# Optimization experiments

Hardware: AMD Instinct MI355X
Metric: run time of the kernel (lower is better)

Reference implementation:

```python
import jax, jax.numpy as jnp
import numpy as np

D_MODEL = 1024
L_MAX = 2048
BATCH = 4
ORDER = 2
FILTER_ORDER = 64
EMB_DIM = 3            # HyenaFilter default positional-embedding dim
SHORT_K = 3
HEAD_DIM = D_MODEL     # num_heads = 1
TOTAL_WIDTH = D_MODEL * (ORDER + 1)
# ExponentialModulation constants (Safari defaults)
MAX_DECAY = np.log(1e-2) / 0.3
MIN_DECAY = np.log(1e-2) / 1.5


def setup_inputs() -> dict:
    key = jax.random.key(0)
    ks = jax.random.split(key, 12)
    s = 0.02
    return {
        "u": jax.random.normal(ks[0], (BATCH, L_MAX, D_MODEL), jnp.float32),
        "in_w": jax.random.normal(ks[1], (D_MODEL, TOTAL_WIDTH), jnp.float32) * s,
        "in_b": jnp.zeros((TOTAL_WIDTH,), jnp.float32),
        "short_w": jax.random.normal(ks[2], (TOTAL_WIDTH, 1, SHORT_K), jnp.float32) * 0.3,
        "short_b": jnp.zeros((TOTAL_WIDTH,), jnp.float32),
        "mlp_w0": jax.random.normal(ks[3], (EMB_DIM, FILTER_ORDER), jnp.float32) * 0.4,
        "mlp_b0": jnp.zeros((FILTER_ORDER,), jnp.float32),
        "freq0": 10.0 * jnp.ones((1, FILTER_ORDER), jnp.float32),
        "mlp_w1": jax.random.normal(ks[4], (FILTER_ORDER, FILTER_ORDER), jnp.float32) * 0.12,
        "mlp_b1": jnp.zeros((FILTER_ORDER,), jnp.float32),
        "freq1": 10.0 * jnp.ones((1, FILTER_ORDER), jnp.float32),
        "mlp_w2": jax.random.normal(ks[5], (FILTER_ORDER, FILTER_ORDER), jnp.float32) * 0.12,
        "mlp_b2": jnp.zeros((FILTER_ORDER,), jnp.float32),
        "freq2": 10.0 * jnp.ones((1, FILTER_ORDER), jnp.float32),
        "mlp_w3": jax.random.normal(ks[6], (FILTER_ORDER, HEAD_DIM), jnp.float32) * 0.1,
        "filter_bias": jax.random.normal(ks[7], (HEAD_DIM,), jnp.float32),
        "out_w": jax.random.normal(ks[8], (D_MODEL, D_MODEL), jnp.float32) * s,
        "out_b": jnp.zeros((D_MODEL,), jnp.float32),
    }


def _pos_emb(L):
    # PositionalEmbedding: t in [0,1], plus exp(-1j * f * w) real/imag bands
    bands = (EMB_DIM - 1) // 2
    t = jnp.linspace(0.0, 1.0, L, dtype=jnp.float32)[:, None]                # (L, 1)
    w = 2.0 * jnp.pi * jnp.linspace(0.0, L - 1.0, L, dtype=jnp.float32)[:, None] / L
    f = jnp.linspace(1e-4, float(bands - 1), bands, dtype=jnp.float32)[None, :]
    phase = f * w                                                             # (L, bands)
    # exp(-1j*phase): real = cos(phase), imag = -sin(phase)
    z = jnp.concatenate([t, jnp.cos(phase), -jnp.sin(phase)], axis=-1)        # (L, EMB_DIM)
    return z, t


def _implicit_filter(L, mlp_w0, mlp_b0, freq0, mlp_w1, mlp_b1, freq1,
                     mlp_w2, mlp_b2, freq2, mlp_w3):
    z, t = _pos_emb(L)
    h = jnp.sin(freq0 * (z @ mlp_w0 + mlp_b0))
    h = jnp.sin(freq1 * (h @ mlp_w1 + mlp_b1))
    h = jnp.sin(freq2 * (h @ mlp_w2 + mlp_b2))
    h = h @ mlp_w3                                                            # (L, HEAD_DIM)
    # ExponentialModulation (shift = 0)
    deltas = jnp.linspace(MIN_DECAY, MAX_DECAY, HEAD_DIM, dtype=jnp.float32)[None, :]
    h = h * jnp.exp(-t * jnp.abs(deltas))
    return h                                                                  # (L, HEAD_DIM)


def _fftconv(u, k, bias):
    # u: (b, v, L), k: (v, L), bias: (v,) -- causal linear conv via 2L FFT
    L = u.shape[-1]
    n = 2 * L
    k_f = jnp.fft.rfft(k, n=n) / n                                            # (v, n//2+1)
    u_f = jnp.fft.rfft(u, n=n)                                                # (b, v, n//2+1)
    y = jnp.fft.irfft(u_f * k_f, n=n, norm="forward")[..., :L]
    return y + u * bias[:, None]


def reference(u, in_w, in_b, short_w, short_b,
              mlp_w0, mlp_b0, freq0, mlp_w1, mlp_b1, freq1,
              mlp_w2, mlp_b2, freq2, mlp_w3, filter_bias, out_w, out_b):
    b, l, d = u.shape
    up = u @ in_w + in_b                                                      # (b, l, 3d)
    up = jnp.transpose(up, (0, 2, 1))                                         # (b, 3d, l)
    # depthwise causal short conv (torch pad=k-1 both sides then [:l] == left pad only)
    uc = jax.lax.conv_general_dilated(
        up, short_w, window_strides=(1,), padding=[(SHORT_K - 1, 0)],
        dimension_numbers=("NCH", "OIH", "NCH"), feature_group_count=TOTAL_WIDTH)
    uc = uc + short_b[None, :, None]                                          # (b, 3d, l)
    x0, x1, v = jnp.split(uc, ORDER + 1, axis=1)                              # each (b, d, l)
    k = _implicit_filter(l, mlp_w0, mlp_b0, freq0, mlp_w1, mlp_b1, freq1,
                         mlp_w2, mlp_b2, freq2, mlp_w3).T                     # (d, l)
    v = v * x1                                                                # gate
    v = _fftconv(v, k, filter_bias)                                           # long conv
    y = jnp.transpose(v * x0, (0, 2, 1))                                      # (b, l, d)
    return y @ out_w + out_b
```

## Files before the change

kernel.cpp:

```cpp
#include <hip/hip_runtime.h>
#include <stdint.h>

typedef unsigned short u16;
typedef __attribute__((ext_vector_type(8))) short short8;
typedef __attribute__((ext_vector_type(4))) short short4x;
typedef __attribute__((ext_vector_type(4))) float f32x4;

#define PI_F 3.14159265358979323846f
#define L_SEQ 2048
#define NFFT 4096
#define DM 1024
#define TW 3072
#define BATCH 4

__device__ __forceinline__ u16 f2bf(float f){
  union { float f; uint32_t u; } v; v.f = f;
  uint32_t r = v.u + 0x7fffu + ((v.u >> 16) & 1u);
  return (u16)(r >> 16);
}
__device__ __forceinline__ float bf2f(u16 h){
  union { uint32_t u; float f; } v; v.u = ((uint32_t)h) << 16;
  return v.f;
}

__device__ __forceinline__ void async16(const void* g, void* l){
  __builtin_amdgcn_global_load_lds(
      (const __attribute__((address_space(1))) void*)g,
      (__attribute__((address_space(3))) void*)l, 16, 0, 0);
}

__device__ __forceinline__ void sincos_rev(float rev, float& sn, float& cs){
  asm("v_sin_f32 %0, %1" : "=v"(sn) : "v"(rev));
  asm("v_cos_f32 %0, %1" : "=v"(cs) : "v"(rev));
}

__device__ __forceinline__ float2 cmulf(float2 a, float c, float s){
  return make_float2(a.x*c - a.y*s, a.x*s + a.y*c);
}

__device__ __forceinline__ int P16(int i){ return i + (i >> 4); }

__device__ static constexpr int BR4[16] = {0,8,4,12,2,10,6,14,1,9,5,13,3,11,7,15};

template<int SGN>
__device__ __forceinline__ void fft16(float2* a){
  const float s = (float)SGN;
  static constexpr float tc[8]  = {1.f, 0.92387953f, 0.70710678f, 0.38268343f,
                                   0.f, -0.38268343f, -0.70710678f, -0.92387953f};
  static constexpr float ts_[8] = {0.f, -0.38268343f, -0.70710678f, -0.92387953f,
                                   -1.f, -0.92387953f, -0.70710678f, -0.38268343f};
  #pragma unroll
  for (int j = 0; j < 8; ++j){
    float2 u = a[j], v = a[j+8];
    float2 d = make_float2(u.x - v.x, u.y - v.y);
    a[j] = make_float2(u.x + v.x, u.y + v.y);
    a[j+8] = cmulf(d, tc[j], s*ts_[j]);
  }
  #pragma unroll
  for (int g = 0; g < 2; ++g){
    int b = g*8;
    #pragma unroll
    for (int j = 0; j < 4; ++j){
      float2 u = a[b+j], v = a[b+j+4];
      float2 d = make_float2(u.x - v.x, u.y - v.y);
      a[b+j] = make_float2(u.x + v.x, u.y + v.y);
      a[b+j+4] = cmulf(d, tc[2*j], s*ts_[2*j]);
    }
  }
  #pragma unroll
  for (int g = 0; g < 4; ++g){
    int b = g*4;
    #pragma unroll
    for (int j = 0; j < 2; ++j){
      float2 u = a[b+j], v = a[b+j+2];
      float2 d = make_float2(u.x - v.x, u.y - v.y);
      a[b+j] = make_float2(u.x + v.x, u.y + v.y);
      a[b+j+2] = (j == 0) ? d : cmulf(d, 0.f, -s);
    }
  }
  #pragma unroll
  for (int g = 0; g < 8; ++g){
    int b = g*2;
    float2 u = a[b], v = a[b+1];
    a[b] = make_float2(u.x + v.x, u.y + v.y);
    a[b+1] = make_float2(u.x - v.x, u.y - v.y);
  }
}

__global__ void k_convert_u(const float4* __restrict__ in, u16* __restrict__ outp, int n4){
  int idx = blockIdx.x * blockDim.x + threadIdx.x;
  int stride = gridDim.x * blockDim.x;
  for (int i = idx; i < n4; i += stride){
    float4 v = in[i];
    u16 r0 = f2bf(v.x), r1 = f2bf(v.y), r2 = f2bf(v.z), r3 = f2bf(v.w);
    u16* o = outp + (size_t)i * 4;
    o[0] = r0; o[1] = r1; o[2] = r2; o[3] = r3;
  }
}

__global__ void k_transpose_w(const float* __restrict__ in, u16* __restrict__ outp, int K, int N){
  __shared__ float tile[32][33];
  int n0 = blockIdx.x * 32, k0 = blockIdx.y * 32;
  int x = threadIdx.x, y = threadIdx.y;
  for (int i = 0; i < 4; ++i)
    tile[y + i*8][x] = in[(size_t)(k0 + y + i*8) * N + n0 + x];
  __syncthreads();
  for (int i = 0; i < 4; ++i)
    outp[(size_t)(n0 + y + i*8) * K + k0 + x] = f2bf(tile[x][y + i*8]);
}

__global__ void k_filter_h2(const float* __restrict__ w0, const float* __restrict__ b0, const float* __restrict__ f0,
                            const float* __restrict__ w1, const float* __restrict__ b1, const float* __restrict__ f1,
                            const float* __restrict__ w2, const float* __restrict__ b2, const float* __restrict__ f2,
                            float* __restrict__ H2T){
  int t = blockIdx.x;
  int j = threadIdx.x;
  float tn = t * (1.0f / 2047.0f);
  float ph = 1e-4f * 2.0f * PI_F * (float)t * (1.0f / 2048.0f);
  float z0 = tn, z1 = cosf(ph), z2 = -sinf(ph);
  __shared__ float hs[64];
  float pre = z0 * w0[j] + z1 * w0[64 + j] + z2 * w0[128 + j] + b0[j];
  float h = sinf(f0[j] * pre);
  hs[j] = h;
  __syncthreads();
  float acc = b1[j];
  for (int i = 0; i < 64; ++i) acc += hs[i] * w1[i*64 + j];
  h = sinf(f1[j] * acc);
  __syncthreads();
  hs[j] = h;
  __syncthreads();
  acc = b2[j];
  for (int i = 0; i < 64; ++i) acc += hs[i] * w2[i*64 + j];
  h = sinf(f2[j] * acc);
  H2T[j * L_SEQ + t] = h;
}

__global__ __launch_bounds__(256) void k_filter_fft16(const float* __restrict__ H2T,
                                                      const float* __restrict__ w3,
                                                      float2* __restrict__ Kf){
  int c0 = blockIdx.x * 2;
  int t = threadIdx.x;
  __shared__ float2 S[4352];
  __shared__ float wcol[2][64];
  if (t < 64){ wcol[0][t] = w3[t * DM + c0]; wcol[1][t] = w3[t * DM + c0 + 1]; }
  __syncthreads();
  const int n1 = t & 15, hi = t >> 4;
  float absd0 = 3.070113457325394f + 12.280453829301576f * ((float)c0 * (1.0f / 1023.0f));
  float absd1 = 3.070113457325394f + 12.280453829301576f * ((float)(c0+1) * (1.0f / 1023.0f));
  float sa[8] = {0,0,0,0,0,0,0,0}, sb[8] = {0,0,0,0,0,0,0,0};
  for (int j = 0; j < 64; ++j){
    float wa = wcol[0][j], wb = wcol[1][j];
    const float* hrow = H2T + j * L_SEQ + t;
    #pragma unroll
    for (int n3 = 0; n3 < 8; ++n3){
      float h = hrow[n3 << 8];
      sa[n3] += h * wa; sb[n3] += h * wb;
    }
  }
  float2 r[16];
  #pragma unroll
  for (int n3 = 0; n3 < 8; ++n3){
    int n = t + (n3 << 8);
    float tn = (float)n * (1.0f / 2047.0f);
    r[n3] = make_float2(sa[n3] * __expf(-tn * absd0), sb[n3] * __expf(-tn * absd1));
    r[n3 + 8] = make_float2(0.f, 0.f);
  }
  fft16<1>(r);
  #pragma unroll
  for (int k3 = 0; k3 < 16; ++k3){
    float sn, cs; sincos_rev(-(float)(hi * k3) * (1.0f/256.0f), sn, cs);
    S[P16(k3*256 + hi*16 + n1)] = cmulf(r[BR4[k3]], cs, sn);
  }
  __syncthreads();
  #pragma unroll
  for (int n2 = 0; n2 < 16; ++n2)
    r[n2] = S[P16(hi*256 + n2*16 + n1)];
  __syncthreads();
  fft16<1>(r);
  #pragma unroll
  for (int k2 = 0; k2 < 16; ++k2){
    float sn, cs; sincos_rev(-(float)(n1 * (hi + 16*k2)) * (1.0f/4096.0f), sn, cs);
    S[P16(k2*256 + hi*16 + n1)] = cmulf(r[BR4[k2]], cs, sn);
  }
  __syncthreads();
  #pragma unroll
  for (int m = 0; m < 16; ++m)
    r[m] = S[P16(hi*256 + n1*16 + m)];
  __syncthreads();
  fft16<1>(r);
  #pragma unroll
  for (int k1 = 0; k1 < 16; ++k1)
    S[P16(t + (k1 << 8))] = r[BR4[k1]];
  __syncthreads();
  const float inv = 1.0f / (float)NFFT;
  float2* kf0 = Kf + (size_t)c0 * NFFT;
  float2* kf1 = kf0 + NFFT;
  int mt = (256 - t) & 255;
  #pragma unroll
  for (int k1 = 0; k1 < 16; ++k1){
    int k = t + (k1 << 8);
    int mk1 = (t == 0) ? ((16 - k1) & 15) : (15 - k1);
    float2 Zk = r[BR4[k1]];
    float2 Zm = S[P16(mt + (mk1 << 8))];
    float gar = 0.5f*(Zk.x + Zm.x), gai = 0.5f*(Zk.y - Zm.y);
    float gbr = 0.5f*(Zk.y + Zm.y), gbi = 0.5f*(Zm.x - Zk.x);
    kf0[k] = make_float2(gar*inv, gai*inv);
    kf1[k] = make_float2(gbr*inv, gbi*inv);
  }
}

__device__ __forceinline__ void gbar(){ __builtin_amdgcn_s_barrier(); }
__device__ __forceinline__ void lgk0(){
  asm volatile("s_waitcnt lgkmcnt(0)" ::: "memory");
  __builtin_amdgcn_sched_barrier(0);
}
template<int V>
__device__ __forceinline__ void waitvm(){
  if constexpr (V == 8) asm volatile("s_waitcnt vmcnt(8)" ::: "memory");
  else if constexpr (V == 6) asm volatile("s_waitcnt vmcnt(6)" ::: "memory");
  else asm volatile("s_waitcnt vmcnt(0)" ::: "memory");
  __builtin_amdgcn_sched_barrier(0);
}

template<int BM, int BN, bool OUT_BF16>
__global__ __launch_bounds__(512, 2) void k_gemm8(const u16* __restrict__ A, const u16* __restrict__ Bt,
                                                  const float* __restrict__ bias, void* __restrict__ Cout,
                                                  int M, int N, int K){
  constexpr int MR  = BM / 32;
  constexpr int NR  = BN / 64;
  constexpr int LA  = BM / 128;
  constexpr int LB  = BN / 128;
  constexpr int V   = 2 * (LA + LB);
  static_assert(LA * 128 == BM && LB * 128 == BN, "stage divisors");
  __shared__ __align__(16) u16 lds[2 * 64 * (BM + BN)];
  const int tid = threadIdx.x;
  const int lane = tid & 63, w = tid >> 6;
  const int wm = w >> 2, wn = w & 3;
  const int lr = lane & 15, lk8 = (lane >> 4) * 8;
  const int NT = K >> 6;

  const int NNT = N / BN;
  int nwg = gridDim.x;
  int swz = (blockIdx.x & 7) * (nwg >> 3) + (blockIdx.x >> 3);
  int m0 = (swz / NNT) * BM;
  int n0 = (swz % NNT) * BN;

  u16* baseA = lds;
  u16* baseB = lds + 2 * 64 * BM;

  auto stageA = [&](int kts, int db, int kh){
    int kc0 = (kts << 6) + kh * 32;
    u16* slab = baseA + db * (BM * 64) + kh * (BM * 32);
    #pragma unroll
    for (int q = 0; q < LA; ++q){
      int row = q * 128 + (tid >> 2);
      int cl = ((tid & 3) * 8) ^ (((row >> 1) & 3) << 3);
      async16(A + (size_t)(m0 + row) * K + kc0 + cl, slab + q * 4096 + (w << 9));
    }
  };
  auto stageB = [&](int kts, int db, int kh){
    int kc0 = (kts << 6) + kh * 32;
    u16* slab = baseB + db * (BN * 64) + kh * (BN * 32);
    #pragma unroll
    for (int q = 0; q < LB; ++q){
      int row = q * 128 + (tid >> 2);
      int cl = ((tid & 3) * 8) ^ (((row >> 1) & 3) << 3);
      async16(Bt + (size_t)(n0 + row) * K + kc0 + cl, slab + q * 4096 + (w << 9));
    }
  };

  f32x4 acc[MR][NR] = {};
  short8 af[MR], bf[NR];

  auto readA = [&](int db, int kh){
    const u16* base = baseA + db * (BM * 64) + kh * (BM * 32);
    #pragma unroll
    for (int i = 0; i < MR; ++i){
      int ar = wm * (BM / 2) + i * 16 + lr;
      af[i] = *(const short8*)&base[ar * 32 + (lk8 ^ (((ar >> 1) & 3) << 3))];
    }
  };
  auto readB = [&](int db, int kh){
    const u16* base = baseB + db * (BN * 64) + kh * (BN * 32);
    #pragma unroll
    for (int j = 0; j < NR; ++j){
      int br = wn * (BN / 4) + j * 16 + lr;
      bf[j] = *(const short8*)&base[br * 32 + (lk8 ^ (((br >> 1) & 3) << 3))];
    }
  };

#define MFMA_FULL                                                              \
  __builtin_amdgcn_s_setprio(1);                                               \
  _Pragma("unroll")                                                            \
  for (int i = 0; i < MR; ++i)                                                 \
    _Pragma("unroll")                                                          \
    for (int j = 0; j < NR; ++j)                                               \
      acc[i][j] = __builtin_amdgcn_mfma_f32_16x16x32_bf16(                     \
          af[i], bf[j], acc[i][j], 0, 0, 0);                                   \
  __builtin_amdgcn_s_setprio(0);

  stageA(0, 0, 0); stageB(0, 0, 0);
  stageA(0, 0, 1); stageB(0, 0, 1);
  stageA(1, 1, 0); stageB(1, 1, 0);
  waitvm<V>();
  gbar();

  for (int kt = 0; kt < NT; ++kt){
    int b = kt & 1, bn2 = b ^ 1;
    int t1 = (kt + 1 < NT) ? kt + 1 : 0;
    int t2 = (kt + 2 < NT) ? kt + 2 : 0;
    readB(b, 0); readA(b, 0);
    stageA(t1, bn2, 1); stageB(t1, bn2, 1);
    gbar(); lgk0();
    MFMA_FULL
    waitvm<V>();
    gbar();
    readB(b, 1); readA(b, 1);
    stageA(t2, b, 0); stageB(t2, b, 0);
    gbar(); lgk0();
    MFMA_FULL
    waitvm<V>();
    gbar();
  }
#undef MFMA_FULL

  waitvm<0>();
  gbar();
  if constexpr (OUT_BF16){
    constexpr int BST = BN + 8;
    u16* lbuf = lds;
    #pragma unroll
    for (int j = 0; j < NR; ++j){
      int col = wn * (BN / 4) + j * 16 + lr;
      float bv = bias[n0 + col];
      #pragma unroll
      for (int i = 0; i < MR; ++i){
        int rw = wm * (BM / 2) + i * 16 + (lane >> 4) * 4;
        #pragma unroll
        for (int r = 0; r < 4; ++r)
          lbuf[(rw + r) * BST + col] = f2bf(acc[i][j][r] + bv);
      }
    }
    gbar();
    constexpr int ROWCH = BN / 8;
    constexpr int CHUNKS = BM * ROWCH;
    #pragma unroll
    for (int q = 0; q < CHUNKS / 512; ++q){
      int c = tid + q * 512;
      int row = c / ROWCH, col8 = (c % ROWCH) * 8;
      f32x4 vv = *(const f32x4*)&lbuf[row * BST + col8];
      *(f32x4*)((u16*)Cout + (size_t)(m0 + row) * N + n0 + col8) = vv;
    }
  } else {
    constexpr int BSTF = BN + 4;
    float* lbuf = (float*)lds;
    constexpr int ROWCHF = BN / 4;
    constexpr int CHUNKSF = (BM / 2) * ROWCHF;
    #pragma unroll
    for (int p = 0; p < 2; ++p){
      if (wm == p){
        #pragma unroll
        for (int j = 0; j < NR; ++j){
          int col = wn * (BN / 4) + j * 16 + lr;
          float bv = bias[n0 + col];
          #pragma unroll
          for (int i = 0; i < MR; ++i){
            int rl = i * 16 + (lane >> 4) * 4;
            #pragma unroll
            for (int r = 0; r < 4; ++r)
              lbuf[(rl + r) * BSTF + col] = acc[i][j][r] + bv;
          }
        }
      }
      gbar();
      #pragma unroll
      for (int q = 0; q < CHUNKSF / 512; ++q){
        int c = tid + q * 512;
        int row = c / ROWCHF, col4 = (c % ROWCHF) * 4;
        f32x4 vv = *(const f32x4*)&lbuf[row * BSTF + col4];
        *(f32x4*)((float*)Cout + (size_t)(m0 + p * (BM / 2) + row) * N + n0 + col4) = vv;
      }
      gbar();
    }
  }
}

__device__ __forceinline__ int ogcol(int c, int t){ return c * 136 + (t ^ (((c >> 3) & 7) << 4)); }

__global__ __launch_bounds__(256) void k_shortconv(const u16* __restrict__ up, const float* __restrict__ sw,
                            const float* __restrict__ sb,
                            u16* __restrict__ gOut, u16* __restrict__ x0Out){
  __shared__ u16 og[2][64 * 136];
  const int t0 = blockIdx.x * 128;
  const int c0 = blockIdx.y * 64;
  const int b  = blockIdx.z;
  const int tid = threadIdx.x;
  const int c8 = (tid & 7) * 8;
  const int tt = (tid >> 3) * 4;
  const int cg = c0 + c8;

  auto conv_group = [&](int g2, float out[8][4]){
    const f32x4* wp = (const f32x4*)(sw + (size_t)(g2 * DM + cg) * 3);
    f32x4 w03 = wp[0], w47 = wp[1], w8b = wp[2], wcf = wp[3], wgj = wp[4], wkn = wp[5];
    float wv[24];
    #pragma unroll
    for (int x = 0; x < 4; ++x){ wv[x] = w03[x]; wv[4+x] = w47[x]; wv[8+x] = w8b[x];
                                 wv[12+x] = wcf[x]; wv[16+x] = wgj[x]; wv[20+x] = wkn[x]; }
    const f32x4* bp = (const f32x4*)(sb + g2 * DM + cg);
    f32x4 b03 = bp[0], b47 = bp[1];
    float bv[8];
    #pragma unroll
    for (int x = 0; x < 4; ++x){ bv[x] = b03[x]; bv[4+x] = b47[x]; }
    const u16* base = up + ((size_t)(b * L_SEQ + t0 + tt - 2)) * TW + g2 * DM + cg;
    short8 rows[6];
    #pragma unroll
    for (int r = 0; r < 6; ++r){
      int t = t0 + tt - 2 + r;
      if (t >= 0) rows[r] = *(const short8*)(base + (size_t)r * TW);
      else rows[r] = (short8)0;
    }
    #pragma unroll
    for (int j = 0; j < 8; ++j){
      float w0 = wv[j*3], w1 = wv[j*3+1], w2 = wv[j*3+2], bb = bv[j];
      #pragma unroll
      for (int q = 0; q < 4; ++q){
        out[j][q] = w0 * bf2f((u16)rows[q][j]) + w1 * bf2f((u16)rows[q+1][j])
                  + w2 * bf2f((u16)rows[q+2][j]) + bb;
      }
    }
  };

  float x1v[8][4], gv[8][4], x0v[8][4];
  conv_group(1, x1v);
  conv_group(2, gv);
  #pragma unroll
  for (int j = 0; j < 8; ++j)
    #pragma unroll
    for (int q = 0; q < 4; ++q) gv[j][q] *= x1v[j][q];
  conv_group(0, x0v);

  #pragma unroll
  for (int j = 0; j < 8; ++j){
    short4x px, pg;
    #pragma unroll
    for (int q = 0; q < 4; ++q){ px[q] = (short)f2bf(x0v[j][q]); pg[q] = (short)f2bf(gv[j][q]); }
    int col = ogcol(c8 + j, tt);
    *(short4x*)&og[0][col] = px;
    *(short4x*)&og[1][col] = pg;
  }
  __syncthreads();

  #pragma unroll
  for (int q = 0; q < 4; ++q){
    int ch = tid + q * 256;
    int c = ch >> 4, t8 = (ch & 15) * 8;
    size_t gb = ((size_t)(b * DM + c0 + c)) * L_SEQ + t0 + t8;
    f32x4 v0 = *(const f32x4*)&og[0][ogcol(c, t8)];
    *(f32x4*)(x0Out + gb) = v0;
    f32x4 v1 = *(const f32x4*)&og[1][ogcol(c, t8)];
    *(f32x4*)(gOut + gb) = v1;
  }
}

__global__ __launch_bounds__(256) void k_fftconv(const u16* __restrict__ g, const u16* __restrict__ x0,
                          const float2* __restrict__ Kf, const float* __restrict__ fbias,
                          u16* __restrict__ z){
  int c0 = blockIdx.x * 2;
  int b = blockIdx.y;
  int t = threadIdx.x;
  __shared__ float2 S[4352];
  const int n1 = t & 15, hi = t >> 4;
  float t1c[16], t1s[16], t2c[16], t2s[16];
  #pragma unroll
  for (int k = 0; k < 16; ++k){
    sincos_rev(-(float)(hi * k) * (1.0f/256.0f), t1s[k], t1c[k]);
    sincos_rev(-(float)(n1 * (hi + 16*k)) * (1.0f/4096.0f), t2s[k], t2c[k]);
  }
  const float2* kf0 = Kf + (size_t)c0 * NFFT;
  const float2* kf1 = kf0 + NFFT;
  const float fb0 = fbias[c0], fb1 = fbias[c0+1];
  const int mt = (256 - t) & 255;
  const size_t row0 = ((size_t)(b * DM + c0)) * L_SEQ;
  const size_t row1 = row0 + L_SEQ;

  float2 r[16];
  #pragma unroll
  for (int n3 = 0; n3 < 8; ++n3){
    int n = t + (n3 << 8);
    r[n3] = make_float2(bf2f(g[row0 + n]), bf2f(g[row1 + n]));
    r[n3 + 8] = make_float2(0.f, 0.f);
  }
  fft16<1>(r);
  #pragma unroll
  for (int k3 = 0; k3 < 16; ++k3)
    S[P16(k3*256 + hi*16 + n1)] = cmulf(r[BR4[k3]], t1c[k3], t1s[k3]);
  __syncthreads();
  #pragma unroll
  for (int n2 = 0; n2 < 16; ++n2)
    r[n2] = S[P16(hi*256 + n2*16 + n1)];
  __syncthreads();
  fft16<1>(r);
  #pragma unroll
  for (int k2 = 0; k2 < 16; ++k2)
    S[P16(k2*256 + hi*16 + n1)] = cmulf(r[BR4[k2]], t2c[k2], t2s[k2]);
  __syncthreads();
  #pragma unroll
  for (int m = 0; m < 16; ++m)
    r[m] = S[P16(hi*256 + n1*16 + m)];
  __syncthreads();
  fft16<1>(r);
  #pragma unroll
  for (int k1 = 0; k1 < 16; ++k1)
    S[P16(t + (k1 << 8))] = r[BR4[k1]];
  __syncthreads();
  float2 y[16];
  #pragma unroll
  for (int k1 = 0; k1 < 16; ++k1){
    int k = t + (k1 << 8);
    int mk1 = (t == 0) ? ((16 - k1) & 15) : (15 - k1);
    float2 Zk = r[BR4[k1]];
    float2 Zm = S[P16(mt + (mk1 << 8))];
    float2 K0 = kf0[k], K1 = kf1[k];
    float gar = 0.5f*(Zk.x + Zm.x), gai = 0.5f*(Zk.y - Zm.y);
    float gbr = 0.5f*(Zk.y + Zm.y), gbi = 0.5f*(Zm.x - Zk.x);
    float yar = gar*K0.x - gai*K0.y, yai = gar*K0.y + gai*K0.x;
    float ybr = gbr*K1.x - gbi*K1.y, ybi = gbr*K1.y + gbi*K1.x;
    y[k1] = make_float2(yar - ybi, yai + ybr);
  }
  fft16<-1>(y);
  __syncthreads();
  #pragma unroll
  for (int n3 = 0; n3 < 16; ++n3)
    S[P16(n3*256 + hi*16 + n1)] = cmulf(y[BR4[n3]], t1c[n3], -t1s[n3]);
  __syncthreads();
  #pragma unroll
  for (int m2 = 0; m2 < 16; ++m2)
    r[m2] = S[P16(hi*256 + m2*16 + n1)];
  __syncthreads();
  fft16<-1>(r);
  #pragma unroll
  for (int nn2 = 0; nn2 < 16; ++nn2)
    S[P16(nn2*256 + hi*16 + n1)] = cmulf(r[BR4[nn2]], t2c[nn2], -t2s[nn2]);
  __syncthreads();
  #pragma unroll
  for (int m = 0; m < 16; ++m)
    r[m] = S[P16(hi*256 + n1*16 + m)];
  fft16<-1>(r);
  #pragma unroll
  for (int q = 0; q < 8; ++q){
    int n = t + (q << 8);
    float2 val = r[BR4[q]];
    float g0 = bf2f(g[row0 + n]), g1 = bf2f(g[row1 + n]);
    float x00 = bf2f(x0[row0 + n]), x01 = bf2f(x0[row1 + n]);
    z[row0 + n] = f2bf((val.x + g0*fb0) * x00);
    z[row1 + n] = f2bf((val.y + g1*fb1) * x01);
  }
}

__global__ __launch_bounds__(256) void k_transpose_z(const u16* __restrict__ zin, u16* __restrict__ zout){
  __shared__ u16 S2[64 * 136];
  const int l0 = blockIdx.x * 64, d0 = blockIdx.y * 64, b = blockIdx.z;
  const int tid = threadIdx.x;
  const int rr = tid >> 3;
  const int ch = tid & 7;
  #pragma unroll
  for (int p = 0; p < 2; ++p){
    int d = rr + p * 32;
    f32x4 v = *(const f32x4*)(zin + ((size_t)(b * DM + d0 + d)) * L_SEQ + l0 + ch * 8);
    *(f32x4*)&S2[d * 136 + ch * 8] = v;
  }
  __syncthreads();
  #pragma unroll
  for (int p = 0; p < 2; ++p){
    int l = rr + p * 32;
    int dc = ch * 8;
    short4x lo, hi2;
    #pragma unroll
    for (int j = 0; j < 4; ++j) lo[j]  = (short)S2[(dc + j) * 136 + l];
    #pragma unroll
    for (int j = 0; j < 4; ++j) hi2[j] = (short)S2[(dc + 4 + j) * 136 + l];
    u16* dst = zout + ((size_t)(b * L_SEQ + l0 + l)) * DM + d0 + dc;
    *(short4x*)dst = lo;
    *(short4x*)(dst + 4) = hi2;
  }
}

extern "C" void kernel_launch(void* const* d_in, const int* in_sizes, int n_in,
                              void* d_out, int out_size, void* d_ws, size_t ws_size,
                              hipStream_t stream){
  (void)in_sizes; (void)n_in; (void)out_size; (void)ws_size;
  const float* u       = (const float*)d_in[0];
  const float* in_w    = (const float*)d_in[1];
  const float* in_b    = (const float*)d_in[2];
  const float* short_w = (const float*)d_in[3];
  const float* short_b = (const float*)d_in[4];
  const float* w0 = (const float*)d_in[5];
  const float* b0 = (const float*)d_in[6];
  const float* f0 = (const float*)d_in[7];
  const float* w1 = (const float*)d_in[8];
  const float* b1 = (const float*)d_in[9];
  const float* f1 = (const float*)d_in[10];
  const float* w2 = (const float*)d_in[11];
  const float* b2 = (const float*)d_in[12];
  const float* f2 = (const float*)d_in[13];
  const float* w3 = (const float*)d_in[14];
  const float* fbias = (const float*)d_in[15];
  const float* out_w = (const float*)d_in[16];
  const float* out_b = (const float*)d_in[17];
  float* out = (float*)d_out;

  char* ws = (char*)d_ws;
  size_t off = 0;
  auto alloc = [&](size_t bytes)->void*{
    void* p = ws + off; off += (bytes + 255) & ~(size_t)255; return p;
  };
  const int M = BATCH * L_SEQ;
  u16*   u_bf  = (u16*)  alloc((size_t)M * DM * 2);
  u16*   inwT  = (u16*)  alloc((size_t)TW * DM * 2);
  u16*   outwT = (u16*)  alloc((size_t)DM * DM * 2);
  float* H2T   = (float*)alloc((size_t)L_SEQ * 64 * 4);
  float2* Kf   = (float2*)alloc((size_t)DM * NFFT * 8);
  u16*   up    = (u16*)  alloc((size_t)M * TW * 2);
  u16*   gbuf  = (u16*)  alloc((size_t)BATCH * DM * L_SEQ * 2);
  u16*   x0buf = (u16*)  alloc((size_t)BATCH * DM * L_SEQ * 2);
  u16*   z  = u_bf;
  u16*   zT = up;

  k_convert_u<<<2048, 256, 0, stream>>>((const float4*)u, u_bf, (M * DM) / 4);
  k_transpose_w<<<dim3(TW/32, DM/32), dim3(32, 8), 0, stream>>>(in_w, inwT, DM, TW);
  k_transpose_w<<<dim3(DM/32, DM/32), dim3(32, 8), 0, stream>>>(out_w, outwT, DM, DM);
  k_filter_h2<<<L_SEQ, 64, 0, stream>>>(w0, b0, f0, w1, b1, f1, w2, b2, f2, H2T);
  k_filter_fft16<<<DM/2, 256, 0, stream>>>(H2T, w3, Kf);
  k_gemm8<128, 384, true><<<dim3((M/128)*(TW/384)), 512, 0, stream>>>(u_bf, inwT, in_b, up, M, TW, DM);
  k_shortconv<<<dim3(L_SEQ/128, DM/64, BATCH), 256, 0, stream>>>(up, short_w, short_b, gbuf, x0buf);
  k_fftconv<<<dim3(DM/2, BATCH), 256, 0, stream>>>(gbuf, x0buf, Kf, fbias, z);
  k_transpose_z<<<dim3(L_SEQ/64, DM/64, BATCH), 256, 0, stream>>>(z, zT);
  k_gemm8<256, 128, false><<<dim3((M/256)*(DM/128)), 512, 0, stream>>>(zT, outwT, out_b, out, M, DM, DM);
}
```

Before: 190.8 us.

## Restructure GEMM into 4-slot half-tile ring pipeline; cache gate values in FFT kernel

The bf16 MFMA GEMM drops its double-buffered two-half-per-iteration loop in favour of a 4-slot ring of 32-wide K phases. Each phase does one wait and one barrier, then issues the stage three phases ahead. The aim is fewer barriers per K step and deeper prefetch, keeping LDS size the same. Separately, the FFT conv kernel keeps the loaded g values in registers instead of reloading them from global memory for the bias term, at the cost of 16 extra registers.

```diff
diff --git a/kernel.cpp b/kernel.cpp
--- a/kernel.cpp
+++ b/kernel.cpp
@@ -230,14 +230,15 @@
   constexpr int NR  = BN / 64;
   constexpr int LA  = BM / 128;
   constexpr int LB  = BN / 128;
-  constexpr int V   = 2 * (LA + LB);
+  constexpr int VW  = 2 * (LA + LB);
   static_assert(LA * 128 == BM && LB * 128 == BN, "stage divisors");
-  __shared__ __align__(16) u16 lds[2 * 64 * (BM + BN)];
+  __shared__ __align__(16) u16 lds[4 * 32 * (BM + BN)];
   const int tid = threadIdx.x;
   const int lane = tid & 63, w = tid >> 6;
   const int wm = w >> 2, wn = w & 3;
   const int lr = lane & 15, lk8 = (lane >> 4) * 8;
   const int NT = K >> 6;
+  const int P  = NT * 2;
 
   const int NNT = N / BN;
   int nwg = gridDim.x;
@@ -246,42 +247,40 @@
   int n0 = (swz % NNT) * BN;
 
   u16* baseA = lds;
-  u16* baseB = lds + 2 * 64 * BM;
-
-  auto stageA = [&](int kts, int db, int kh){
-    int kc0 = (kts << 6) + kh * 32;
-    u16* slab = baseA + db * (BM * 64) + kh * (BM * 32);
+  u16* baseB = lds + 4 * BM * 32;
+
+  auto stagePhase = [&](int p){
+    int kt = p >> 1, kh = p & 1, sl = p & 3;
+    int kc0 = (kt << 6) + kh * 32;
+    u16* slabA = baseA + sl * (BM * 32);
     #pragma unroll
     for (int q = 0; q < LA; ++q){
       int row = q * 128 + (tid >> 2);
       int cl = ((tid & 3) * 8) ^ (((row >> 1) & 3) << 3);
-      async16(A + (size_t)(m0 + row) * K + kc0 + cl, slab + q * 4096 + (w << 9));
-    }
-  };
-  auto stageB = [&](int kts, int db, int kh){
-    int kc0 = (kts << 6) + kh * 32;
-    u16* slab = baseB + db * (BN * 64) + kh * (BN * 32);
+      async16(A + (size_t)(m0 + row) * K + kc0 + cl, slabA + q * 4096 + (w << 9));
+    }
+    u16* slabB = baseB + sl * (BN * 32);
     #pragma unroll
     for (int q = 0; q < LB; ++q){
       int row = q * 128 + (tid >> 2);
       int cl = ((tid & 3) * 8) ^ (((row >> 1) & 3) << 3);
-      async16(Bt + (size_t)(n0 + row) * K + kc0 + cl, slab + q * 4096 + (w << 9));
+      async16(Bt + (size_t)(n0 + row) * K + kc0 + cl, slabB + q * 4096 + (w << 9));
     }
   };
 
   f32x4 acc[MR][NR] = {};
   short8 af[MR], bf[NR];
 
-  auto readA = [&](int db, int kh){
-    const u16* base = baseA + db * (BM * 64) + kh * (BM * 32);
+  auto readA = [&](int sl){
+    const u16* base = baseA + sl * (BM * 32);
     #pragma unroll
     for (int i = 0; i < MR; ++i){
       int ar = wm * (BM / 2) + i * 16 + lr;
       af[i] = *(const short8*)&base[ar * 32 + (lk8 ^ (((ar >> 1) & 3) << 3))];
     }
   };
-  auto readB = [&](int db, int kh){
-    const u16* base = baseB + db * (BN * 64) + kh * (BN * 32);
+  auto readB = [&](int sl){
+    const u16* base = baseB + sl * (BN * 32);
     #pragma unroll
     for (int j = 0; j < NR; ++j){
       int br = wn * (BN / 4) + j * 16 + lr;
@@ -289,40 +288,24 @@
     }
   };
 
-#define MFMA_FULL                                                              \
-  __builtin_amdgcn_s_setprio(1);                                               \
-  _Pragma("unroll")                                                            \
-  for (int i = 0; i < MR; ++i)                                                 \
-    _Pragma("unroll")                                                          \
-    for (int j = 0; j < NR; ++j)                                               \
-      acc[i][j] = __builtin_amdgcn_mfma_f32_16x16x32_bf16(                     \
-          af[i], bf[j], acc[i][j], 0, 0, 0);                                   \
-  __builtin_amdgcn_s_setprio(0);
-
-  stageA(0, 0, 0); stageB(0, 0, 0);
-  stageA(0, 0, 1); stageB(0, 0, 1);
-  stageA(1, 1, 0); stageB(1, 1, 0);
-  waitvm<V>();
-  gbar();
-
-  for (int kt = 0; kt < NT; ++kt){
-    int b = kt & 1, bn2 = b ^ 1;
-    int t1 = (kt + 1 < NT) ? kt + 1 : 0;
-    int t2 = (kt + 2 < NT) ? kt + 2 : 0;
-    readB(b, 0); readA(b, 0);
-    stageA(t1, bn2, 1); stageB(t1, bn2, 1);
-    gbar(); lgk0();
-    MFMA_FULL
-    waitvm<V>();
+  stagePhase(0); stagePhase(1); stagePhase(2);
+
+  for (int p = 0; p < P; ++p){
+    waitvm<VW>();
     gbar();
-    readB(b, 1); readA(b, 1);
-    stageA(t2, b, 0); stageB(t2, b, 0);
-    gbar(); lgk0();
-    MFMA_FULL
-    waitvm<V>();
-    gbar();
-  }
-#undef MFMA_FULL
+    int sl = p & 3;
+    readB(sl); readA(sl);
+    int pt = p + 3; if (pt >= P) pt -= P;
+    stagePhase(pt);
+    lgk0();
+    __builtin_amdgcn_s_setprio(1);
+    #pragma unroll
+    for (int i = 0; i < MR; ++i)
+      #pragma unroll
+      for (int j = 0; j < NR; ++j)
+        acc[i][j] = __builtin_amdgcn_mfma_f32_16x16x32_bf16(af[i], bf[j], acc[i][j], 0, 0, 0);
+    __builtin_amdgcn_s_setprio(0);
+  }
 
   waitvm<0>();
   gbar();
@@ -357,8 +340,8 @@
     constexpr int ROWCHF = BN / 4;
     constexpr int CHUNKSF = (BM / 2) * ROWCHF;
     #pragma unroll
-    for (int p = 0; p < 2; ++p){
-      if (wm == p){
+    for (int p2 = 0; p2 < 2; ++p2){
+      if (wm == p2){
         #pragma unroll
         for (int j = 0; j < NR; ++j){
           int col = wn * (BN / 4) + j * 16 + lr;
@@ -378,7 +361,7 @@
         int c = tid + q * 512;
         int row = c / ROWCHF, col4 = (c % ROWCHF) * 4;
         f32x4 vv = *(const f32x4*)&lbuf[row * BSTF + col4];
-        *(f32x4*)((float*)Cout + (size_t)(m0 + p * (BM / 2) + row) * N + n0 + col4) = vv;
+        *(f32x4*)((float*)Cout + (size_t)(m0 + p2 * (BM / 2) + row) * N + n0 + col4) = vv;
       }
       gbar();
     }
@@ -484,10 +467,13 @@
   const size_t row1 = row0 + L_SEQ;
 
   float2 r[16];
+  float gv0[8], gv1[8];
   #pragma unroll
   for (int n3 = 0; n3 < 8; ++n3){
     int n = t + (n3 << 8);
-    r[n3] = make_float2(bf2f(g[row0 + n]), bf2f(g[row1 + n]));
+    float a0 = bf2f(g[row0 + n]), a1 = bf2f(g[row1 + n]);
+    gv0[n3] = a0; gv1[n3] = a1;
+    r[n3] = make_float2(a0, a1);
     r[n3 + 8] = make_float2(0.f, 0.f);
   }
   fft16<1>(r);
@@ -550,10 +536,9 @@
   for (int q = 0; q < 8; ++q){
     int n = t + (q << 8);
     float2 val = r[BR4[q]];
-    float g0 = bf2f(g[row0 + n]), g1 = bf2f(g[row1 + n]);
     float x00 = bf2f(x0[row0 + n]), x01 = bf2f(x0[row1 + n]);
-    z[row0 + n] = f2bf((val.x + g0*fb0) * x00);
-    z[row1 + n] = f2bf((val.y + g1*fb1) * x01);
+    z[row0 + n] = f2bf((val.x + gv0[q]*fb0) * x00);
+    z[row1 + n] = f2bf((val.y + gv1[q]*fb1) * x01);
   }
 }
 
```

Measured after the change: 195.2 us. +2.3%, slower.
